# Performance work log

Measured on AMD Instinct MI355X. Metric: run time of the kernel, lower is better.

The kernel has to match this reference:

```python
import jax, jax.numpy as jnp
import numpy as np

E = 1024  # embed_dim
R = 16    # LoRA rank
B = 4
S = 2048


def setup_inputs() -> dict:
    key = jax.random.key(0)
    ks = jax.random.split(key, 12)
    inp = {
        'query': jax.random.normal(ks[0], (B, S, E), jnp.float32),
        'key': jax.random.normal(ks[1], (B, S, E), jnp.float32),
        'value': jax.random.normal(ks[2], (B, S, E), jnp.float32),
        'Q_weight': jax.random.normal(ks[3], (E, E), jnp.float32) / np.sqrt(E),
        'K_weight': jax.random.normal(ks[4], (E, E), jnp.float32) / np.sqrt(E),
        'V_weight': jax.random.normal(ks[5], (E, E), jnp.float32) / np.sqrt(E),
        'Q_A': 0.02 * jax.random.normal(ks[6], (R, E), jnp.float32),
        'Q_B': 0.02 * jax.random.normal(ks[7], (E, R), jnp.float32),
        'K_A': 0.02 * jax.random.normal(ks[8], (R, E), jnp.float32),
        'K_B': 0.02 * jax.random.normal(ks[9], (E, R), jnp.float32),
        'V_A': 0.02 * jax.random.normal(ks[10], (R, E), jnp.float32),
        'V_B': 0.02 * jax.random.normal(ks[11], (E, R), jnp.float32),
        'O_weight': jax.random.normal(jax.random.fold_in(key, 99), (E, E), jnp.float32) / np.sqrt(E),
    }
    return inp


def reference(query, key, value, Q_weight, K_weight, V_weight,
              Q_A, Q_B, K_A, K_B, V_A, V_B, O_weight):
    embed_dim = Q_weight.shape[0]
    # base projections (linear(x, W) = x @ W.T) + low-rank LoRA deltas
    Q = jnp.einsum('bse,fe->bsf', query, Q_weight) + jnp.einsum('bse,re->bsr', query, Q_A) @ Q_B.T
    K = jnp.einsum('bse,fe->bsf', key, K_weight) + jnp.einsum('bse,re->bsr', key, K_A) @ K_B.T
    V = jnp.einsum('bse,fe->bsf', value, V_weight) + jnp.einsum('bse,re->bsr', value, V_A) @ V_B.T
    scores = jnp.einsum('bqe,bke->bqk', Q, K) / jnp.sqrt(jnp.float32(embed_dim))
    attn = jax.nn.softmax(scores, axis=-1)
    out = jnp.einsum('bqk,bke->bqe', attn, V)
    return jnp.einsum('bse,fe->bsf', out, O_weight)
```

## Files before the change

kernel.cpp:

```cpp
#include <hip/hip_runtime.h>


#define S_LEN 2048
#define E_DIM 1024

typedef __attribute__((ext_vector_type(8))) short short8;
typedef __attribute__((ext_vector_type(4))) float floatx4;

__device__ __forceinline__ unsigned short f2bf(float f) {
  union { float f; unsigned int u; } x; x.f = f;
  return (unsigned short)((x.u + 0x7fffu + ((x.u >> 16) & 1u)) >> 16);
}
__device__ __forceinline__ float bf2f(unsigned short h) {
  union { unsigned int u; float f; } x; x.u = ((unsigned int)h) << 16;
  return x.f;
}

__device__ __forceinline__ void gld_lds16(const unsigned short* g, unsigned short* l) {
  __builtin_amdgcn_global_load_lds(
      (const __attribute__((address_space(1))) unsigned int*)(const void*)g,
      (__attribute__((address_space(3))) unsigned int*)(void*)l,
      16, 0, 0);
}

template<bool LORA, bool OUTF32, bool OWNM>
__global__ __launch_bounds__(512, 2) void gemm8p(
    const unsigned short* __restrict__ A, const unsigned short* __restrict__ B,
    void* __restrict__ Cv,
    const unsigned short* __restrict__ LA, const unsigned short* __restrict__ LB,
    long lda, long ldb, long ldc, int K, float scale,
    long batA, long batB, long batC, long batLA, long batLB) {
  __shared__ alignas(16) unsigned short As[2][2][8192];
  __shared__ alignas(16) unsigned short Bs[2][2][8192];

  const int tid  = threadIdx.x;
  const int wave = tid >> 6, lane = tid & 63;
  const int quad = lane >> 4, l16 = lane & 15;
  const int wr = wave >> 2, wc = wave & 3;

  const int Nx = (int)gridDim.x, Ny = (int)gridDim.y;
  const int wg2 = (int)blockIdx.x + Nx * (int)blockIdx.y;
  const int xcd = wg2 & 7, ii = wg2 >> 3;
  int bx, by;
  if constexpr (OWNM) {
    const int lg = 31 - __clz(Nx);
    by = xcd * (Ny >> 3) + (ii >> lg);
    bx = ii & (Nx - 1);
  } else {
    const int lg = 31 - __clz(Ny);
    bx = xcd * (Nx >> 3) + (ii >> lg);
    by = ii & (Ny - 1);
  }
  const long m0 = (long)by * 256;
  const long n0 = (long)bx * 256;
  const unsigned short* Az = A + (long)blockIdx.z * batA;
  const unsigned short* Bz = B + (long)blockIdx.z * batB;

  floatx4 acc[8][4];
#pragma unroll
  for (int i = 0; i < 8; ++i)
#pragma unroll
    for (int j = 0; j < 4; ++j) acc[i][j] = (floatx4){0.f, 0.f, 0.f, 0.f};

  const int lr = tid >> 3;
  const int sp = (tid & 7) ^ (lr & 7);
  const unsigned short* aS = Az + (m0 + lr) * lda + sp * 8;
  const unsigned short* bS = Bz + (n0 + (lr >> 5) * 64 + (lr & 31)) * ldb + sp * 8;

#define STG_A(bf, F, k0)                                                     \
  do {                                                                       \
    gld_lds16(aS + (long)((F) * 64) * lda + (k0), &As[bf][F][tid * 8]);      \
    gld_lds16(aS + (long)((F) * 64 + 128) * lda + (k0),                      \
              &As[bf][F][4096 + tid * 8]);                                   \
  } while (0)
#define STG_B(bf, G, k0)                                                     \
  do {                                                                       \
    gld_lds16(bS + (long)((G) * 32) * ldb + (k0), &Bs[bf][G][tid * 8]);      \
    gld_lds16(bS + (long)((G) * 32 + 128) * ldb + (k0),                      \
              &Bs[bf][G][4096 + tid * 8]);                                   \
  } while (0)

  const int xo    = (l16 & 7) << 4;
  const int aoff0 = ((quad * 16) ^ xo) >> 1;
  const int aoff1 = ((64 + quad * 16) ^ xo) >> 1;
  const int arow  = wr * 4096 + l16 * 64;
  const int brow  = wc * 2048 + l16 * 64;

  STG_A(0, 0, 0); STG_B(0, 0, 0); STG_A(0, 1, 0); STG_B(0, 1, 0);

  const int NT = K >> 6;
  for (int t = 0; t < NT; ++t) {
    const int cur = t & 1, nbf = cur ^ 1;
    const int kN = (t + 1 < NT ? t + 1 : NT - 1) << 6;
    short8 aLo[4][2], aHi[4][2], b0f[2][2], b1f[2][2];

    asm volatile("s_waitcnt vmcnt(4)\n\ts_barrier" ::: "memory");
#pragma unroll
    for (int i = 0; i < 4; ++i) {
      aLo[i][0] = *(const short8*)&As[cur][0][arow + i * 1024 + aoff0];
      aLo[i][1] = *(const short8*)&As[cur][0][arow + i * 1024 + aoff1];
    }
#pragma unroll
    for (int j = 0; j < 2; ++j) {
      b0f[j][0] = *(const short8*)&Bs[cur][0][brow + j * 1024 + aoff0];
      b0f[j][1] = *(const short8*)&Bs[cur][0][brow + j * 1024 + aoff1];
    }
    STG_A(nbf, 0, kN);
    asm volatile("s_waitcnt lgkmcnt(0)" ::: "memory");
    __builtin_amdgcn_s_setprio(1);
#pragma unroll
    for (int ks = 0; ks < 2; ++ks)
#pragma unroll
      for (int i = 0; i < 4; ++i)
#pragma unroll
        for (int j = 0; j < 2; ++j)
          acc[i][j] = __builtin_amdgcn_mfma_f32_16x16x32_bf16(
              aLo[i][ks], b0f[j][ks], acc[i][j], 0, 0, 0);
    __builtin_amdgcn_s_setprio(0);

    asm volatile("s_waitcnt vmcnt(4)\n\ts_barrier" ::: "memory");
#pragma unroll
    for (int i = 0; i < 4; ++i) {
      aHi[i][0] = *(const short8*)&As[cur][1][arow + i * 1024 + aoff0];
      aHi[i][1] = *(const short8*)&As[cur][1][arow + i * 1024 + aoff1];
    }
    STG_B(nbf, 0, kN);
    asm volatile("s_waitcnt lgkmcnt(0)" ::: "memory");
    __builtin_amdgcn_s_setprio(1);
#pragma unroll
    for (int ks = 0; ks < 2; ++ks)
#pragma unroll
      for (int i = 0; i < 4; ++i)
#pragma unroll
        for (int j = 0; j < 2; ++j)
          acc[i + 4][j] = __builtin_amdgcn_mfma_f32_16x16x32_bf16(
              aHi[i][ks], b0f[j][ks], acc[i + 4][j], 0, 0, 0);
    __builtin_amdgcn_s_setprio(0);

    asm volatile("s_waitcnt vmcnt(4)\n\ts_barrier" ::: "memory");
#pragma unroll
    for (int j = 0; j < 2; ++j) {
      b1f[j][0] = *(const short8*)&Bs[cur][1][brow + j * 1024 + aoff0];
      b1f[j][1] = *(const short8*)&Bs[cur][1][brow + j * 1024 + aoff1];
    }
    STG_A(nbf, 1, kN);
    asm volatile("s_waitcnt lgkmcnt(0)" ::: "memory");
    __builtin_amdgcn_s_setprio(1);
#pragma unroll
    for (int ks = 0; ks < 2; ++ks)
#pragma unroll
      for (int i = 0; i < 4; ++i)
#pragma unroll
        for (int j = 0; j < 2; ++j)
          acc[i][j + 2] = __builtin_amdgcn_mfma_f32_16x16x32_bf16(
              aLo[i][ks], b1f[j][ks], acc[i][j + 2], 0, 0, 0);
    __builtin_amdgcn_s_setprio(0);

    __builtin_amdgcn_s_barrier();
    STG_B(nbf, 1, kN);
    __builtin_amdgcn_s_setprio(1);
#pragma unroll
    for (int ks = 0; ks < 2; ++ks)
#pragma unroll
      for (int i = 0; i < 4; ++i)
#pragma unroll
        for (int j = 0; j < 2; ++j)
          acc[i + 4][j + 2] = __builtin_amdgcn_mfma_f32_16x16x32_bf16(
              aHi[i][ks], b1f[j][ks], acc[i + 4][j + 2], 0, 0, 0);
    __builtin_amdgcn_s_setprio(0);
  }

  asm volatile("s_waitcnt vmcnt(0)" ::: "memory");

  if constexpr (LORA) {
    const unsigned short* LAz = LA + (long)blockIdx.z * batLA;
    const unsigned short* LBz = LB + (long)blockIdx.z * batLB;
    const short8 z8 = {0, 0, 0, 0, 0, 0, 0, 0};
    short8 b2[4];
#pragma unroll
    for (int j = 0; j < 4; ++j) {
      const long row = n0 + wc * 64 + j * 16 + l16;
      b2[j] = (quad < 2) ? *(const short8*)(LBz + row * 16 + quad * 8) : z8;
    }
#pragma unroll
    for (int i = 0; i < 8; ++i) {
      const long row = m0 + wr * 128 + i * 16 + l16;
      const short8 a2 =
          (quad < 2) ? *(const short8*)(LAz + row * 16 + quad * 8) : z8;
#pragma unroll
      for (int j = 0; j < 4; ++j)
        acc[i][j] = __builtin_amdgcn_mfma_f32_16x16x32_bf16(a2, b2[j], acc[i][j], 0, 0, 0);
    }
  }

#pragma unroll
  for (int i = 0; i < 8; ++i) {
    const long row = m0 + wr * 128 + i * 16 + quad * 4;
#pragma unroll
    for (int j = 0; j < 4; ++j) {
      const long col = n0 + wc * 64 + j * 16 + l16;
#pragma unroll
      for (int rr = 0; rr < 4; ++rr) {
        float val = acc[i][j][rr] * scale;
        if constexpr (OUTF32)
          ((float*)Cv)[(long)blockIdx.z * batC + (row + rr) * ldc + col] = val;
        else
          ((unsigned short*)Cv)[(long)blockIdx.z * batC + (row + rr) * ldc + col] = f2bf(val);
      }
    }
  }
#undef STG_A
#undef STG_B
}

__device__ __forceinline__ uint4 pack8(const float* x) {
  float4 a = *(const float4*)x;
  float4 b = *(const float4*)(x + 4);
  uint4 o;
  o.x = (unsigned int)f2bf(a.x) | ((unsigned int)f2bf(a.y) << 16);
  o.y = (unsigned int)f2bf(a.z) | ((unsigned int)f2bf(a.w) << 16);
  o.z = (unsigned int)f2bf(b.x) | ((unsigned int)f2bf(b.y) << 16);
  o.w = (unsigned int)f2bf(b.z) | ((unsigned int)f2bf(b.w) << 16);
  return o;
}

__global__ __launch_bounds__(256) void prep_qkv(
    const float* __restrict__ q, const float* __restrict__ k, const float* __restrict__ v,
    unsigned short* __restrict__ qb, unsigned short* __restrict__ kb,
    unsigned short* __restrict__ vb) {
  const float* X; unsigned short* Y;
  if (blockIdx.y == 0)      { X = q; Y = qb; }
  else if (blockIdx.y == 1) { X = k; Y = kb; }
  else                      { X = v; Y = vb; }
  const int tid = threadIdx.x;
  const long blk = (long)blockIdx.x * 16384;
#pragma unroll
  for (int it = 0; it < 8; ++it) {
    const long idx = blk + it * 2048 + tid * 8;
    *(uint4*)(Y + idx) = pack8(X + idx);
  }
}

__global__ __launch_bounds__(256) void cvt_all(
    const float* __restrict__ Wq, const float* __restrict__ Wk,
    const float* __restrict__ Wv, const float* __restrict__ Wo,
    const float* __restrict__ QB, const float* __restrict__ KB, const float* __restrict__ VB,
    const float* __restrict__ QA, const float* __restrict__ KA, const float* __restrict__ VA,
    unsigned short* __restrict__ wqb, unsigned short* __restrict__ wkb,
    unsigned short* __restrict__ wvb, unsigned short* __restrict__ wob,
    unsigned short* __restrict__ Bqb, unsigned short* __restrict__ Bkb, unsigned short* __restrict__ Bvb,
    unsigned short* __restrict__ Aqb, unsigned short* __restrict__ Akb, unsigned short* __restrict__ Avb) {
  if (blockIdx.y < 4) {
    const float* x; unsigned short* y;
    switch (blockIdx.y) {
      case 0: x = Wq; y = wqb; break;
      case 1: x = Wk; y = wkb; break;
      case 2: x = Wv; y = wvb; break;
      default: x = Wo; y = wob; break;
    }
    const long i = ((long)blockIdx.x * 256 + threadIdx.x) * 8;
    *(uint4*)(y + i) = pack8(x + i);
  } else {
    if (blockIdx.x >= 48) return;
    const int mat = blockIdx.x >> 3, sub = blockIdx.x & 7;
    const float* x; unsigned short* y;
    switch (mat) {
      case 0: x = QB; y = Bqb; break;
      case 1: x = KB; y = Bkb; break;
      case 2: x = VB; y = Bvb; break;
      case 3: x = QA; y = Aqb; break;
      case 4: x = KA; y = Akb; break;
      default: x = VA; y = Avb; break;
    }
    const long i = ((long)sub * 256 + threadIdx.x) * 8;
    *(uint4*)(y + i) = pack8(x + i);
  }
}

__global__ __launch_bounds__(256) void lora_t_mfma(
    const unsigned short* __restrict__ qb, const unsigned short* __restrict__ kb,
    const unsigned short* __restrict__ vb,
    const unsigned short* __restrict__ Aq, const unsigned short* __restrict__ Ak,
    const unsigned short* __restrict__ Av,
    unsigned short* __restrict__ Tq, unsigned short* __restrict__ Tk,
    unsigned short* __restrict__ Tv) {
  const unsigned short* X; const unsigned short* Am; unsigned short* T;
  if (blockIdx.y == 0)      { X = qb; Am = Aq; T = Tq; }
  else if (blockIdx.y == 1) { X = kb; Am = Ak; T = Tk; }
  else                      { X = vb; Am = Av; T = Tv; }
  const int tid = threadIdx.x, wave = tid >> 6, lane = tid & 63;
  const int quad = lane >> 4, l16 = lane & 15;
  const long m0 = (long)blockIdx.x * 64 + wave * 16;
  floatx4 acc = (floatx4){0.f, 0.f, 0.f, 0.f};
  const unsigned short* xp = X + (m0 + l16) * 1024 + quad * 8;
  const unsigned short* ap = Am + (long)l16 * 1024 + quad * 8;
#pragma unroll 4
  for (int k0 = 0; k0 < 1024; k0 += 32) {
    short8 af = *(const short8*)(xp + k0);
    short8 bf = *(const short8*)(ap + k0);
    acc = __builtin_amdgcn_mfma_f32_16x16x32_bf16(af, bf, acc, 0, 0, 0);
  }
#pragma unroll
  for (int rr = 0; rr < 4; ++rr)
    T[(m0 + quad * 4 + rr) * 16 + l16] = f2bf(acc[rr]);
}

__global__ __launch_bounds__(256) void softmax_kernel(unsigned short* __restrict__ S) {
  const long base = (long)blockIdx.x * 2048;
  const int tid = threadIdx.x;
  const int lane = tid & 63, wave = tid >> 6;
  __shared__ float redm[4], reds[4];
  uint4 raw = *(const uint4*)(S + base + tid * 8);
  unsigned int w[4] = {raw.x, raw.y, raw.z, raw.w};
  float v[8];
#pragma unroll
  for (int i = 0; i < 4; ++i) {
    v[2 * i]     = bf2f((unsigned short)(w[i] & 0xffffu));
    v[2 * i + 1] = bf2f((unsigned short)(w[i] >> 16));
  }
  float m = v[0];
#pragma unroll
  for (int i = 1; i < 8; ++i) m = fmaxf(m, v[i]);
  for (int off = 32; off >= 1; off >>= 1) m = fmaxf(m, __shfl_xor(m, off, 64));
  if (lane == 0) redm[wave] = m;
  __syncthreads();
  m = fmaxf(fmaxf(redm[0], redm[1]), fmaxf(redm[2], redm[3]));
  float e[8], s = 0.f;
#pragma unroll
  for (int i = 0; i < 8; ++i) { e[i] = __expf(v[i] - m); s += e[i]; }
  for (int off = 32; off >= 1; off >>= 1) s += __shfl_xor(s, off, 64);
  if (lane == 0) reds[wave] = s;
  __syncthreads();
  s = reds[0] + reds[1] + reds[2] + reds[3];
  const float inv = 1.0f / s;
  uint4 o;
  o.x = (unsigned int)f2bf(e[0] * inv) | ((unsigned int)f2bf(e[1] * inv) << 16);
  o.y = (unsigned int)f2bf(e[2] * inv) | ((unsigned int)f2bf(e[3] * inv) << 16);
  o.z = (unsigned int)f2bf(e[4] * inv) | ((unsigned int)f2bf(e[5] * inv) << 16);
  o.w = (unsigned int)f2bf(e[6] * inv) | ((unsigned int)f2bf(e[7] * inv) << 16);
  *(uint4*)(S + base + tid * 8) = o;
}

extern "C" void kernel_launch(void* const* d_in, const int* in_sizes, int n_in,
                              void* d_out, int out_size, void* d_ws, size_t ws_size,
                              hipStream_t stream) {
  const float* q  = (const float*)d_in[0];
  const float* k  = (const float*)d_in[1];
  const float* v  = (const float*)d_in[2];
  const float* Wq = (const float*)d_in[3];
  const float* Wk = (const float*)d_in[4];
  const float* Wv = (const float*)d_in[5];
  const float* QA = (const float*)d_in[6];
  const float* QB = (const float*)d_in[7];
  const float* KA = (const float*)d_in[8];
  const float* KB = (const float*)d_in[9];
  const float* VA = (const float*)d_in[10];
  const float* VB = (const float*)d_in[11];
  const float* Wo = (const float*)d_in[12];

  unsigned short* W = (unsigned short*)d_ws;
  const long SEe = (long)8192 * 1024;
  unsigned short* qb  = W;
  unsigned short* kb  = W + SEe;
  unsigned short* vb  = W + 2 * SEe;
  unsigned short* Qp  = W + 3 * SEe;
  unsigned short* Kp  = W + 4 * SEe;
  unsigned short* VT  = W + 5 * SEe;
  unsigned short* wqb = W + 6 * SEe;
  unsigned short* wkb = wqb + 1048576;
  unsigned short* wvb = wkb + 1048576;
  unsigned short* wob = wvb + 1048576;
  unsigned short* Bqb = wob + 1048576;
  unsigned short* Bkb = Bqb + 16384;
  unsigned short* Bvb = Bkb + 16384;
  unsigned short* Aqb = Bvb + 16384;
  unsigned short* Akb = Aqb + 16384;
  unsigned short* Avb = Akb + 16384;
  unsigned short* Tq  = Avb + 16384;
  unsigned short* Tk  = Tq + 131072;
  unsigned short* Tv  = Tk + 131072;
  unsigned short* scores = W;
  unsigned short* attn   = vb;

  dim3 blk(256, 1, 1), blk5(512, 1, 1);
  prep_qkv<<<dim3(512, 3, 1), blk, 0, stream>>>(q, k, v, qb, kb, vb);
  cvt_all<<<dim3(512, 5, 1), blk, 0, stream>>>(Wq, Wk, Wv, Wo, QB, KB, VB, QA, KA, VA,
                                               wqb, wkb, wvb, wob, Bqb, Bkb, Bvb, Aqb, Akb, Avb);
  lora_t_mfma<<<dim3(128, 3, 1), blk, 0, stream>>>(qb, kb, vb, Aqb, Akb, Avb, Tq, Tk, Tv);

  gemm8p<true, false, true><<<dim3(4, 32, 2), blk5, 0, stream>>>(
      qb, wqb, Qp, Tq, Bqb, 1024, 1024, 1024, 1024, 1.0f,
      SEe, 1048576, SEe, 131072, 16384);
  gemm8p<true, false, false><<<dim3(32, 4, 1), blk5, 0, stream>>>(
      wvb, vb, VT, Bvb, Tv, 1024, 1024, 8192, 1024, 1.0f, 0, 0, 0, 0, 0);
  gemm8p<false, false, true><<<dim3(8, 8, 4), blk5, 0, stream>>>(
      Qp, Kp, scores, nullptr, nullptr, 1024, 1024, 2048, 1024, 0.03125f,
      (long)S_LEN * E_DIM, (long)S_LEN * E_DIM, (long)S_LEN * S_LEN, 0, 0);
  softmax_kernel<<<8192, blk, 0, stream>>>(scores);
  gemm8p<false, false, true><<<dim3(4, 8, 4), blk5, 0, stream>>>(
      scores, VT, attn, nullptr, nullptr, 2048, 8192, 1024, 2048, 1.0f,
      (long)S_LEN * S_LEN, (long)S_LEN, (long)S_LEN * E_DIM, 0, 0);
  gemm8p<false, true, true><<<dim3(4, 32, 1), blk5, 0, stream>>>(
      attn, wob, d_out, nullptr, nullptr, 1024, 1024, 1024, 1024, 1.0f, 0, 0, 0, 0, 0);
}
```

Before: 380.3 us.

## Restructure GEMM main loop to prefetch LDS fragments and add 128-row tile variant

The main loop of the 256x256 GEMM is reordered. All eight global-to-LDS loads for the next K-step are issued together, and the next step's A-low/B0 fragments are read from LDS during the current step's last MFMA block, so fewer barriers and waits sit between LDS reads and MFMAs. A new gemm128 kernel uses a 128x256 tile with launch_bounds(512,2). It replaces gemm8p for the V projection, attn@V and output projection, doubling the workgroup count on small grids to improve CU fill. The cost is a smaller tile with less reuse per byte loaded, and more register pressure from holding fragments across barriers.

```diff
diff --git a/kernel.cpp b/kernel.cpp
--- a/kernel.cpp
+++ b/kernel.cpp
@@ -67,17 +67,16 @@
   const unsigned short* aS = Az + (m0 + lr) * lda + sp * 8;
   const unsigned short* bS = Bz + (n0 + (lr >> 5) * 64 + (lr & 31)) * ldb + sp * 8;
 
-#define STG_A(bf, F, k0)                                                     \
-  do {                                                                       \
-    gld_lds16(aS + (long)((F) * 64) * lda + (k0), &As[bf][F][tid * 8]);      \
-    gld_lds16(aS + (long)((F) * 64 + 128) * lda + (k0),                      \
-              &As[bf][F][4096 + tid * 8]);                                   \
-  } while (0)
-#define STG_B(bf, G, k0)                                                     \
-  do {                                                                       \
-    gld_lds16(bS + (long)((G) * 32) * ldb + (k0), &Bs[bf][G][tid * 8]);      \
-    gld_lds16(bS + (long)((G) * 32 + 128) * ldb + (k0),                      \
-              &Bs[bf][G][4096 + tid * 8]);                                   \
+#define STAGE8(bf, k0)                                                       \
+  do {                                                                       \
+    gld_lds16(aS + (k0), &As[bf][0][tid * 8]);                               \
+    gld_lds16(aS + (long)128 * lda + (k0), &As[bf][0][4096 + tid * 8]);      \
+    gld_lds16(bS + (k0), &Bs[bf][0][tid * 8]);                               \
+    gld_lds16(bS + (long)128 * ldb + (k0), &Bs[bf][0][4096 + tid * 8]);      \
+    gld_lds16(aS + (long)64 * lda + (k0), &As[bf][1][tid * 8]);              \
+    gld_lds16(aS + (long)192 * lda + (k0), &As[bf][1][4096 + tid * 8]);      \
+    gld_lds16(bS + (long)32 * ldb + (k0), &Bs[bf][1][tid * 8]);              \
+    gld_lds16(bS + (long)160 * ldb + (k0), &Bs[bf][1][4096 + tid * 8]);      \
   } while (0)
 
   const int xo    = (l16 & 7) << 4;
@@ -86,91 +85,75 @@
   const int arow  = wr * 4096 + l16 * 64;
   const int brow  = wc * 2048 + l16 * 64;
 
-  STG_A(0, 0, 0); STG_B(0, 0, 0); STG_A(0, 1, 0); STG_B(0, 1, 0);
+  short8 aLo[4][2], aHi[4][2], b0f[2][2], b1f[2][2];
+
+#define READ_ALO(bf)                                                         \
+  do {                                                                       \
+    _Pragma("unroll") for (int i = 0; i < 4; ++i) {                          \
+      aLo[i][0] = *(const short8*)&As[bf][0][arow + i * 1024 + aoff0];       \
+      aLo[i][1] = *(const short8*)&As[bf][0][arow + i * 1024 + aoff1];       \
+    }                                                                        \
+  } while (0)
+#define READ_AHI(bf)                                                         \
+  do {                                                                       \
+    _Pragma("unroll") for (int i = 0; i < 4; ++i) {                          \
+      aHi[i][0] = *(const short8*)&As[bf][1][arow + i * 1024 + aoff0];       \
+      aHi[i][1] = *(const short8*)&As[bf][1][arow + i * 1024 + aoff1];       \
+    }                                                                        \
+  } while (0)
+#define READ_B0(bf)                                                          \
+  do {                                                                       \
+    _Pragma("unroll") for (int j = 0; j < 2; ++j) {                          \
+      b0f[j][0] = *(const short8*)&Bs[bf][0][brow + j * 1024 + aoff0];       \
+      b0f[j][1] = *(const short8*)&Bs[bf][0][brow + j * 1024 + aoff1];       \
+    }                                                                        \
+  } while (0)
+#define READ_B1(bf)                                                          \
+  do {                                                                       \
+    _Pragma("unroll") for (int j = 0; j < 2; ++j) {                          \
+      b1f[j][0] = *(const short8*)&Bs[bf][1][brow + j * 1024 + aoff0];       \
+      b1f[j][1] = *(const short8*)&Bs[bf][1][brow + j * 1024 + aoff1];       \
+    }                                                                        \
+  } while (0)
+#define QUAD(am, bm, io, jo)                                                 \
+  do {                                                                       \
+    _Pragma("unroll") for (int ks = 0; ks < 2; ++ks)                         \
+      _Pragma("unroll") for (int i = 0; i < 4; ++i)                          \
+        _Pragma("unroll") for (int j = 0; j < 2; ++j)                        \
+          acc[i + (io)][j + (jo)] = __builtin_amdgcn_mfma_f32_16x16x32_bf16( \
+              am[i][ks], bm[j][ks], acc[i + (io)][j + (jo)], 0, 0, 0);       \
+  } while (0)
+
+  STAGE8(0, 0);
+  asm volatile("s_waitcnt vmcnt(0)\n\ts_barrier" ::: "memory");
+  READ_ALO(0); READ_B0(0);
 
   const int NT = K >> 6;
   for (int t = 0; t < NT; ++t) {
     const int cur = t & 1, nbf = cur ^ 1;
     const int kN = (t + 1 < NT ? t + 1 : NT - 1) << 6;
-    short8 aLo[4][2], aHi[4][2], b0f[2][2], b1f[2][2];
-
-    asm volatile("s_waitcnt vmcnt(4)\n\ts_barrier" ::: "memory");
-#pragma unroll
-    for (int i = 0; i < 4; ++i) {
-      aLo[i][0] = *(const short8*)&As[cur][0][arow + i * 1024 + aoff0];
-      aLo[i][1] = *(const short8*)&As[cur][0][arow + i * 1024 + aoff1];
-    }
-#pragma unroll
-    for (int j = 0; j < 2; ++j) {
-      b0f[j][0] = *(const short8*)&Bs[cur][0][brow + j * 1024 + aoff0];
-      b0f[j][1] = *(const short8*)&Bs[cur][0][brow + j * 1024 + aoff1];
-    }
-    STG_A(nbf, 0, kN);
-    asm volatile("s_waitcnt lgkmcnt(0)" ::: "memory");
+
+    asm volatile("s_barrier" ::: "memory");
+    READ_AHI(cur); READ_B1(cur);
+    STAGE8(nbf, kN);
     __builtin_amdgcn_s_setprio(1);
-#pragma unroll
-    for (int ks = 0; ks < 2; ++ks)
-#pragma unroll
-      for (int i = 0; i < 4; ++i)
-#pragma unroll
-        for (int j = 0; j < 2; ++j)
-          acc[i][j] = __builtin_amdgcn_mfma_f32_16x16x32_bf16(
-              aLo[i][ks], b0f[j][ks], acc[i][j], 0, 0, 0);
+    QUAD(aLo, b0f, 0, 0);
     __builtin_amdgcn_s_setprio(0);
 
-    asm volatile("s_waitcnt vmcnt(4)\n\ts_barrier" ::: "memory");
-#pragma unroll
-    for (int i = 0; i < 4; ++i) {
-      aHi[i][0] = *(const short8*)&As[cur][1][arow + i * 1024 + aoff0];
-      aHi[i][1] = *(const short8*)&As[cur][1][arow + i * 1024 + aoff1];
-    }
-    STG_B(nbf, 0, kN);
-    asm volatile("s_waitcnt lgkmcnt(0)" ::: "memory");
+    asm volatile("s_barrier" ::: "memory");
     __builtin_amdgcn_s_setprio(1);
-#pragma unroll
-    for (int ks = 0; ks < 2; ++ks)
-#pragma unroll
-      for (int i = 0; i < 4; ++i)
-#pragma unroll
-        for (int j = 0; j < 2; ++j)
-          acc[i + 4][j] = __builtin_amdgcn_mfma_f32_16x16x32_bf16(
-              aHi[i][ks], b0f[j][ks], acc[i + 4][j], 0, 0, 0);
+    QUAD(aHi, b0f, 4, 0);
+    QUAD(aLo, b1f, 0, 2);
     __builtin_amdgcn_s_setprio(0);
-
-    asm volatile("s_waitcnt vmcnt(4)\n\ts_barrier" ::: "memory");
-#pragma unroll
-    for (int j = 0; j < 2; ++j) {
-      b1f[j][0] = *(const short8*)&Bs[cur][1][brow + j * 1024 + aoff0];
-      b1f[j][1] = *(const short8*)&Bs[cur][1][brow + j * 1024 + aoff1];
-    }
-    STG_A(nbf, 1, kN);
-    asm volatile("s_waitcnt lgkmcnt(0)" ::: "memory");
+    asm volatile("s_waitcnt vmcnt(4)" ::: "memory");
+
+    asm volatile("s_barrier" ::: "memory");
+    READ_ALO(nbf); READ_B0(nbf);
     __builtin_amdgcn_s_setprio(1);
-#pragma unroll
-    for (int ks = 0; ks < 2; ++ks)
-#pragma unroll
-      for (int i = 0; i < 4; ++i)
-#pragma unroll
-        for (int j = 0; j < 2; ++j)
-          acc[i][j + 2] = __builtin_amdgcn_mfma_f32_16x16x32_bf16(
-              aLo[i][ks], b1f[j][ks], acc[i][j + 2], 0, 0, 0);
+    QUAD(aHi, b1f, 4, 2);
     __builtin_amdgcn_s_setprio(0);
-
-    __builtin_amdgcn_s_barrier();
-    STG_B(nbf, 1, kN);
-    __builtin_amdgcn_s_setprio(1);
-#pragma unroll
-    for (int ks = 0; ks < 2; ++ks)
-#pragma unroll
-      for (int i = 0; i < 4; ++i)
-#pragma unroll
-        for (int j = 0; j < 2; ++j)
-          acc[i + 4][j + 2] = __builtin_amdgcn_mfma_f32_16x16x32_bf16(
-              aHi[i][ks], b1f[j][ks], acc[i + 4][j + 2], 0, 0, 0);
-    __builtin_amdgcn_s_setprio(0);
-  }
-
-  asm volatile("s_waitcnt vmcnt(0)" ::: "memory");
+    asm volatile("s_waitcnt vmcnt(0)" ::: "memory");
+  }
 
   if constexpr (LORA) {
     const unsigned short* LAz = LA + (long)blockIdx.z * batLA;
@@ -209,8 +192,172 @@
       }
     }
   }
-#undef STG_A
-#undef STG_B
+#undef STAGE8
+#undef READ_ALO
+#undef READ_AHI
+#undef READ_B0
+#undef READ_B1
+#undef QUAD
+}
+
+template<bool LORA, bool OUTF32, bool OWNM>
+__global__ __launch_bounds__(512, 2) void gemm128(
+    const unsigned short* __restrict__ A, const unsigned short* __restrict__ B,
+    void* __restrict__ Cv,
+    const unsigned short* __restrict__ LA, const unsigned short* __restrict__ LB,
+    long lda, long ldb, long ldc, int K, float scale,
+    long batA, long batB, long batC, long batLA, long batLB) {
+  __shared__ alignas(16) unsigned short As[2][2][4096];
+  __shared__ alignas(16) unsigned short Bs[2][2][8192];
+
+  const int tid  = threadIdx.x;
+  const int wave = tid >> 6, lane = tid & 63;
+  const int quad = lane >> 4, l16 = lane & 15;
+  const int wr = wave >> 2, wc = wave & 3;
+
+  const int Nx = (int)gridDim.x, Ny = (int)gridDim.y;
+  const int wg2 = (int)blockIdx.x + Nx * (int)blockIdx.y;
+  const int xcd = wg2 & 7, ii = wg2 >> 3;
+  int bx, by;
+  if constexpr (OWNM) {
+    const int lg = 31 - __clz(Nx);
+    by = xcd * (Ny >> 3) + (ii >> lg);
+    bx = ii & (Nx - 1);
+  } else {
+    const int lg = 31 - __clz(Ny);
+    bx = xcd * (Nx >> 3) + (ii >> lg);
+    by = ii & (Ny - 1);
+  }
+  const long m0 = (long)by * 128;
+  const long n0 = (long)bx * 256;
+  const unsigned short* Az = A + (long)blockIdx.z * batA;
+  const unsigned short* Bz = B + (long)blockIdx.z * batB;
+
+  floatx4 acc[4][4];
+#pragma unroll
+  for (int i = 0; i < 4; ++i)
+#pragma unroll
+    for (int j = 0; j < 4; ++j) acc[i][j] = (floatx4){0.f, 0.f, 0.f, 0.f};
+
+  const int lr = tid >> 3;
+  const int sp = (tid & 7) ^ (lr & 7);
+  const unsigned short* aS = Az + (m0 + (lr >> 5) * 64 + (lr & 31)) * lda + sp * 8;
+  const unsigned short* bS  = Bz + (n0 + (lr >> 5) * 64 + (lr & 31)) * ldb + sp * 8;
+  const unsigned short* bS2 = Bz + (n0 + ((lr + 64) >> 5) * 64 + ((lr + 64) & 31)) * ldb + sp * 8;
+
+#define STAGE6(bf, k0)                                                       \
+  do {                                                                       \
+    gld_lds16(aS + (k0), &As[bf][0][tid * 8]);                               \
+    gld_lds16(bS + (k0), &Bs[bf][0][tid * 8]);                               \
+    gld_lds16(bS2 + (k0), &Bs[bf][0][4096 + tid * 8]);                       \
+    gld_lds16(aS + (long)32 * lda + (k0), &As[bf][1][tid * 8]);              \
+    gld_lds16(bS + (long)32 * ldb + (k0), &Bs[bf][1][tid * 8]);              \
+    gld_lds16(bS2 + (long)32 * ldb + (k0), &Bs[bf][1][4096 + tid * 8]);      \
+  } while (0)
+
+  const int xo    = (l16 & 7) << 4;
+  const int aoff0 = ((quad * 16) ^ xo) >> 1;
+  const int aoff1 = ((64 + quad * 16) ^ xo) >> 1;
+  const int arow  = wr * 2048 + l16 * 64;
+  const int brow  = wc * 2048 + l16 * 64;
+
+  short8 aF0[2][2], aF1[2][2], bG0[2][2], bG1[2][2];
+
+#define READ_AF(ar, h)                                                       \
+  do {                                                                       \
+    _Pragma("unroll") for (int i = 0; i < 2; ++i) {                          \
+      ar[i][0] = *(const short8*)&As[bf_][h][arow + i * 1024 + aoff0];       \
+      ar[i][1] = *(const short8*)&As[bf_][h][arow + i * 1024 + aoff1];       \
+    }                                                                        \
+  } while (0)
+#define READ_BG(br, h)                                                       \
+  do {                                                                       \
+    _Pragma("unroll") for (int j = 0; j < 2; ++j) {                          \
+      br[j][0] = *(const short8*)&Bs[bf_][h][brow + j * 1024 + aoff0];       \
+      br[j][1] = *(const short8*)&Bs[bf_][h][brow + j * 1024 + aoff1];       \
+    }                                                                        \
+  } while (0)
+#define QUAD(am, bm, io, jo)                                                 \
+  do {                                                                       \
+    _Pragma("unroll") for (int ks = 0; ks < 2; ++ks)                         \
+      _Pragma("unroll") for (int i = 0; i < 2; ++i)                          \
+        _Pragma("unroll") for (int j = 0; j < 2; ++j)                        \
+          acc[i + (io)][j + (jo)] = __builtin_amdgcn_mfma_f32_16x16x32_bf16( \
+              am[i][ks], bm[j][ks], acc[i + (io)][j + (jo)], 0, 0, 0);       \
+  } while (0)
+
+  STAGE6(0, 0);
+  asm volatile("s_waitcnt vmcnt(0)\n\ts_barrier" ::: "memory");
+  { const int bf_ = 0; READ_AF(aF0, 0); READ_BG(bG0, 0); }
+
+  const int NT = K >> 6;
+  for (int t = 0; t < NT; ++t) {
+    const int cur = t & 1, nbf = cur ^ 1;
+    const int kN = (t + 1 < NT ? t + 1 : NT - 1) << 6;
+
+    asm volatile("s_barrier" ::: "memory");
+    { const int bf_ = cur; READ_AF(aF1, 1); READ_BG(bG1, 1); }
+    STAGE6(nbf, kN);
+    __builtin_amdgcn_s_setprio(1);
+    QUAD(aF0, bG0, 0, 0);
+    __builtin_amdgcn_s_setprio(0);
+
+    asm volatile("s_barrier" ::: "memory");
+    __builtin_amdgcn_s_setprio(1);
+    QUAD(aF1, bG0, 2, 0);
+    QUAD(aF0, bG1, 0, 2);
+    __builtin_amdgcn_s_setprio(0);
+    asm volatile("s_waitcnt vmcnt(3)" ::: "memory");
+
+    asm volatile("s_barrier" ::: "memory");
+    { const int bf_ = nbf; READ_AF(aF0, 0); READ_BG(bG0, 0); }
+    __builtin_amdgcn_s_setprio(1);
+    QUAD(aF1, bG1, 2, 2);
+    __builtin_amdgcn_s_setprio(0);
+    asm volatile("s_waitcnt vmcnt(0)" ::: "memory");
+  }
+
+  if constexpr (LORA) {
+    const unsigned short* LAz = LA + (long)blockIdx.z * batLA;
+    const unsigned short* LBz = LB + (long)blockIdx.z * batLB;
+    const short8 z8 = {0, 0, 0, 0, 0, 0, 0, 0};
+    short8 b2[4];
+#pragma unroll
+    for (int j = 0; j < 4; ++j) {
+      const long row = n0 + wc * 64 + j * 16 + l16;
+      b2[j] = (quad < 2) ? *(const short8*)(LBz + row * 16 + quad * 8) : z8;
+    }
+#pragma unroll
+    for (int i = 0; i < 4; ++i) {
+      const long row = m0 + wr * 64 + i * 16 + l16;
+      const short8 a2 =
+          (quad < 2) ? *(const short8*)(LAz + row * 16 + quad * 8) : z8;
+#pragma unroll
+      for (int j = 0; j < 4; ++j)
+        acc[i][j] = __builtin_amdgcn_mfma_f32_16x16x32_bf16(a2, b2[j], acc[i][j], 0, 0, 0);
+    }
+  }
+
+#pragma unroll
+  for (int i = 0; i < 4; ++i) {
+    const long row = m0 + wr * 64 + i * 16 + quad * 4;
+#pragma unroll
+    for (int j = 0; j < 4; ++j) {
+      const long col = n0 + wc * 64 + j * 16 + l16;
+#pragma unroll
+      for (int rr = 0; rr < 4; ++rr) {
+        float val = acc[i][j][rr] * scale;
+        if constexpr (OUTF32)
+          ((float*)Cv)[(long)blockIdx.z * batC + (row + rr) * ldc + col] = val;
+        else
+          ((unsigned short*)Cv)[(long)blockIdx.z * batC + (row + rr) * ldc + col] = f2bf(val);
+      }
+    }
+  }
+#undef STAGE6
+#undef READ_AF
+#undef READ_BG
+#undef QUAD
 }
 
 __device__ __forceinline__ uint4 pack8(const float* x) {
@@ -391,15 +538,15 @@
   gemm8p<true, false, true><<<dim3(4, 32, 2), blk5, 0, stream>>>(
       qb, wqb, Qp, Tq, Bqb, 1024, 1024, 1024, 1024, 1.0f,
       SEe, 1048576, SEe, 131072, 16384);
-  gemm8p<true, false, false><<<dim3(32, 4, 1), blk5, 0, stream>>>(
+  gemm128<true, false, false><<<dim3(32, 8, 1), blk5, 0, stream>>>(
       wvb, vb, VT, Bvb, Tv, 1024, 1024, 8192, 1024, 1.0f, 0, 0, 0, 0, 0);
   gemm8p<false, false, true><<<dim3(8, 8, 4), blk5, 0, stream>>>(
       Qp, Kp, scores, nullptr, nullptr, 1024, 1024, 2048, 1024, 0.03125f,
       (long)S_LEN * E_DIM, (long)S_LEN * E_DIM, (long)S_LEN * S_LEN, 0, 0);
   softmax_kernel<<<8192, blk, 0, stream>>>(scores);
-  gemm8p<false, false, true><<<dim3(4, 8, 4), blk5, 0, stream>>>(
+  gemm128<false, false, true><<<dim3(4, 16, 4), blk5, 0, stream>>>(
       scores, VT, attn, nullptr, nullptr, 2048, 8192, 1024, 2048, 1.0f,
       (long)S_LEN * S_LEN, (long)S_LEN, (long)S_LEN * E_DIM, 0, 0);
-  gemm8p<false, true, true><<<dim3(4, 32, 1), blk5, 0, stream>>>(
+  gemm128<false, true, true><<<dim3(4, 64, 1), blk5, 0, stream>>>(
       attn, wob, d_out, nullptr, nullptr, 1024, 1024, 1024, 1024, 1.0f, 0, 0, 0, 0, 0);
 }
```

Result: faster. 360.7 us (-5.2%).
